# Kernel optimization log

Measured on AMD Instinct MI355X. Metric: run time of the kernel, lower is better.

## Reference

```python
import jax, jax.numpy as jnp
import numpy as np

B, C, H, W = 4, 256, 96, 96
HEADS, RATE = 8, 1


def setup_inputs() -> dict:
    key = jax.random.key(0)
    ks = [jax.random.fold_in(key, i) for i in range(8)]
    kpe = 2 * (RATE // 2) + 1  # PE depthwise kernel size (1 for rate=1)
    return {
        "q": jax.random.normal(ks[0], (B, C, H, W), jnp.float32),
        "k": jax.random.normal(ks[1], (B, C, H, W), jnp.float32),
        "v": jax.random.normal(ks[2], (B, C, H, W), jnp.float32),
        "wq": jax.random.normal(ks[3], (C, C), jnp.float32) * 0.02,          # q_proj 1x1 (used for q,k,v per source)
        "pe_dw": jax.random.normal(ks[4], (9, 1, kpe, kpe), jnp.float32) * 0.3,  # grouped conv, groups=9
        "pe_pw": jax.random.normal(ks[5], (9, 9, 1, 1), jnp.float32) * 0.3,      # 1x1 mixing conv
        "wo": jax.random.normal(ks[6], (C, C), jnp.float32) * 0.02,          # out_proj weight
        "bo": jax.random.normal(ks[7], (C,), jnp.float32) * 0.02,            # out_proj bias
    }


def _unfold3(x, rate):
    # torch.nn.Unfold(3, dilation=rate, padding=rate) then view(N, c, 9, H, W)
    # kernel positions are row-major (ki, kj), channel-major layout -> stack on axis 2.
    n, c, h, w = x.shape
    xp = jnp.pad(x, ((0, 0), (0, 0), (rate, rate), (rate, rate)))
    pats = [xp[:, :, i * rate:i * rate + h, j * rate:j * rate + w]
            for i in range(3) for j in range(3)]
    return jnp.stack(pats, axis=2)  # (N, c, 9, H, W)


def reference(q, b_unused_k=None, v=None, wq=None, pe_dw=None, pe_pw=None, wo=None, bo=None, k=None):
    raise NotImplementedError  # replaced below


def reference(q, k, v, wq, pe_dw, pe_pw, wo, bo):
    b = q.shape[0]
    ch = C // HEADS
    proj = lambda x: jnp.einsum('oc,bchw->bohw', wq, x)  # source uses q_proj for q, k AND v
    qh = proj(q).reshape(b * HEADS, ch, H, W)
    kh = proj(k).reshape(b * HEADS, ch, H, W)
    vh = proj(v).reshape(b * HEADS, ch, H, W)

    ku = _unfold3(kh, RATE)                              # (bH, ch, 9, H, W)
    f = jnp.einsum('nchw,nckhw->nkhw', qh, ku)           # per-pixel 3x3 scores (bH, 9, H, W)

    pad = RATE // 2
    dn = ('NCHW', 'OIHW', 'NCHW')
    f = jax.lax.conv_general_dilated(f, pe_dw, (1, 1), [(pad, pad), (pad, pad)],
                                     feature_group_count=9, dimension_numbers=dn)
    f = jax.lax.conv_general_dilated(f, pe_pw, (1, 1), 'VALID', dimension_numbers=dn)
    s = jax.nn.softmax(f, axis=1)                        # softmax over 9 kernel positions

    vu = _unfold3(vh, RATE)                              # (bH, ch, 9, H, W)
    o = jnp.einsum('nckhw,nkhw->nchw', vu, s).reshape(b, C, H, W)
    return jnp.einsum('oc,bchw->bohw', wo, o) + bo[None, :, None, None]
```

## Files before the change

### kernel.cpp

```cpp
#include <hip/hip_runtime.h>
#include <math.h>

#define HH 96
#define WW 96
#define PP 9216
#define CCH 256
#define BB 4
#define CH 32

typedef unsigned short u16;
typedef short bf16x8 __attribute__((ext_vector_type(8)));
typedef float f32x4 __attribute__((ext_vector_type(4)));

__device__ __forceinline__ float bf2f(unsigned s) { return __uint_as_float(s << 16); }
__device__ __forceinline__ u16 f2bf(float f) {
  unsigned u = __float_as_uint(f);
  return (u16)((u + 0x7fffu + ((u >> 16) & 1u)) >> 16);
}

typedef __attribute__((address_space(1))) const unsigned int GUI;
typedef __attribute__((address_space(3))) unsigned int LUI;
__device__ __forceinline__ void gload16(const void* g, void* l) {
  __builtin_amdgcn_global_load_lds((GUI*)g, (LUI*)l, 16, 0, 0);
}

__global__ __launch_bounds__(256)
void wcvt(const float* __restrict__ wq, const float* __restrict__ wo,
          u16* __restrict__ Wbf) {
  int gidx = blockIdx.x * 256 + threadIdx.x;
  int mat = gidx >> 13;
  int gi = gidx & 8191;
  int l = gi & 63;
  int i = (gi >> 6) & 3;
  int w = (gi >> 8) & 3;
  int ks = (gi >> 10) & 1;
  int kk = (gi >> 11) & 3;
  const float* W = mat ? wo : wq;
  int row = w * 64 + i * 16 + (l & 15);
  int c0 = kk * 64 + (ks * 4 + (l >> 4)) * 8;
  const float* s = W + (size_t)row * CCH + c0;
  float4 a = *(const float4*)s;
  float4 b = *(const float4*)(s + 4);
  uint4 u;
  u.x = (unsigned)f2bf(a.x) | ((unsigned)f2bf(a.y) << 16);
  u.y = (unsigned)f2bf(a.z) | ((unsigned)f2bf(a.w) << 16);
  u.z = (unsigned)f2bf(b.x) | ((unsigned)f2bf(b.y) << 16);
  u.w = (unsigned)f2bf(b.z) | ((unsigned)f2bf(b.w) << 16);
  *(uint4*)(Wbf + (size_t)gidx * 8) = u;
}

#define TSTR 68
__global__ __launch_bounds__(256, 3)
void gemm_qkvf(const float* __restrict__ qin, const float* __restrict__ kin,
               const float* __restrict__ vin, const u16* __restrict__ Wbf,
               u16* __restrict__ Xcl) {
  __shared__ float Tt[2][64][TSTR];
  const int t = threadIdx.x;
  const int w = t >> 6, l = t & 63;
  const int lr = l & 15, lg = l >> 4;
  const int pblk = blockIdx.x * 64;
  const int z = blockIdx.z;
  const int b = z & 3, which = z >> 2;
  const float* Xf = ((which == 0) ? qin : (which == 1) ? kin : vin) + (size_t)b * CCH * PP;
  u16* Y = Xcl + (size_t)z * ((size_t)PP * CCH);

  const int sw_r = ((lr >> 2) & 3) << 3;
  const int cswz = (lr & 3) << 3;

  f32x4 acc[4][4];
#pragma unroll
  for (int mi = 0; mi < 4; mi++)
#pragma unroll
    for (int ni = 0; ni < 4; ni++) acc[mi][ni] = (f32x4){0.f, 0.f, 0.f, 0.f};

  float4 xr[4];
  auto loadX = [&](int kk) {
#pragma unroll
    for (int rr = 0; rr < 4; rr++) {
      int cc = kk * 64 + w * 4 + lg + 16 * rr;
      xr[rr] = *(const float4*)(Xf + (size_t)cc * PP + pblk + lr * 4);
    }
  };
  auto writeT = [&](int buf) {
#pragma unroll
    for (int rr = 0; rr < 4; rr++) {
      int cs = (w * 4 + lg + 16 * rr) ^ cswz;
      Tt[buf][lr * 4 + 0][cs] = xr[rr].x;
      Tt[buf][lr * 4 + 1][cs] = xr[rr].y;
      Tt[buf][lr * 4 + 2][cs] = xr[rr].z;
      Tt[buf][lr * 4 + 3][cs] = xr[rr].w;
    }
  };
  auto mma = [&](int kk, int cur) {
#pragma unroll
    for (int ks = 0; ks < 2; ks++) {
      bf16x8 wf[4], xf[4];
#pragma unroll
      for (int i = 0; i < 4; i++) {
        size_t go = ((((size_t)(kk * 2 + ks) * 4 + w) * 4 + i) * 64 + l) * 8;
        wf[i] = *(const bf16x8*)(Wbf + go);
      }
#pragma unroll
      for (int i = 0; i < 4; i++) {
        int row = i * 16 + lr;
        int c0 = (ks * 32 + lg * 8) ^ sw_r;
        const float* tp = &Tt[cur][row][c0];
        float4 A = *(const float4*)tp;
        float4 Bv = *(const float4*)(tp + 4);
        bf16x8 x;
        x[0] = (short)f2bf(A.x);  x[1] = (short)f2bf(A.y);
        x[2] = (short)f2bf(A.z);  x[3] = (short)f2bf(A.w);
        x[4] = (short)f2bf(Bv.x); x[5] = (short)f2bf(Bv.y);
        x[6] = (short)f2bf(Bv.z); x[7] = (short)f2bf(Bv.w);
        xf[i] = x;
      }
#pragma unroll
      for (int mi = 0; mi < 4; mi++)
#pragma unroll
        for (int ni = 0; ni < 4; ni++)
          acc[mi][ni] = __builtin_amdgcn_mfma_f32_16x16x32_bf16(
              wf[mi], xf[ni], acc[mi][ni], 0, 0, 0);
    }
  };

  loadX(0);
  writeT(0);
  __syncthreads();
#pragma unroll
  for (int kk = 0; kk < 4; kk++) {
    if (kk < 3) loadX(kk + 1);
    mma(kk, kk & 1);
    if (kk < 3) {
      writeT((kk + 1) & 1);
      __syncthreads();
    }
  }

#pragma unroll
  for (int mi = 0; mi < 4; mi++)
#pragma unroll
    for (int ni = 0; ni < 4; ni++) {
      int o = w * 64 + mi * 16 + lg * 4;
      int p = pblk + ni * 16 + lr;
      f32x4 a = acc[mi][ni];
      uint2 u;
      u.x = (unsigned)f2bf(a[0]) | ((unsigned)f2bf(a[1]) << 16);
      u.y = (unsigned)f2bf(a[2]) | ((unsigned)f2bf(a[3]) << 16);
      *(uint2*)(Y + (size_t)p * CCH + o) = u;
    }
}

__global__ __launch_bounds__(256)
void gemm_out_m(const u16* __restrict__ Xbuf, const u16* __restrict__ Wbf,
                const float* __restrict__ bias, float* __restrict__ outY) {
  __shared__ u16 Xl[64 * 64];
  const int t = threadIdx.x;
  const int w = t >> 6, l = t & 63;
  const int lr = l & 15, lg = l >> 4;
  const int pblk = blockIdx.x * 64;
  const int z = blockIdx.z;
  const u16* Xb = Xbuf + (size_t)z * ((size_t)PP * CCH);

  f32x4 acc[4][4];
#pragma unroll
  for (int mi = 0; mi < 4; mi++)
#pragma unroll
    for (int ni = 0; ni < 4; ni++) acc[mi][ni] = (f32x4){0.f, 0.f, 0.f, 0.f};

  for (int kk = 0; kk < 4; kk++) {
    const int c0 = kk * 64;
#pragma unroll
    for (int i = 0; i < 2; i++) {
      int r0 = (w * 2 + i) * 8;
      int row = r0 + (l >> 3);
      int gs = (l & 7) ^ (row & 7);
      gload16(Xb + (size_t)(pblk + row) * CCH + c0 + gs * 8, (void*)&Xl[r0 * 64]);
    }
    __syncthreads();
#pragma unroll
    for (int ks = 0; ks < 2; ks++) {
      const int g = ks * 4 + lg;
      bf16x8 wf[4], xf[4];
#pragma unroll
      for (int i = 0; i < 4; i++) {
        size_t go = ((((size_t)(kk * 2 + ks) * 4 + w) * 4 + i) * 64 + l) * 8;
        wf[i] = *(const bf16x8*)(Wbf + go);
      }
#pragma unroll
      for (int i = 0; i < 4; i++) {
        int row = i * 16 + lr;
        xf[i] = *(const bf16x8*)&Xl[row * 64 + ((g ^ (row & 7)) << 3)];
      }
#pragma unroll
      for (int mi = 0; mi < 4; mi++)
#pragma unroll
        for (int ni = 0; ni < 4; ni++)
          acc[mi][ni] = __builtin_amdgcn_mfma_f32_16x16x32_bf16(
              xf[mi], wf[ni], acc[mi][ni], 0, 0, 0);
    }
    __syncthreads();
  }
#pragma unroll
  for (int ni = 0; ni < 4; ni++) {
    int o = w * 64 + ni * 16 + lr;
    float bv = bias[o];
#pragma unroll
    for (int mi = 0; mi < 4; mi++) {
      int p = pblk + mi * 16 + lg * 4;
      f32x4 a = acc[mi][ni];
      float4 st = {a[0] + bv, a[1] + bv, a[2] + bv, a[3] + bv};
      *(float4*)(outY + ((size_t)z * CCH + o) * PP + p) = st;
    }
  }
}

#define TX 32
#define TY 4
#define HX 34
#define HY 6
#define NHP (HX * HY)
#define NGR (NHP * 4)
#define ARND 4

__device__ __forceinline__ void fma8(const uint4 u, const float* qp, float& s) {
  s = fmaf(qp[0], bf2f(u.x & 0xffffu), s);
  s = fmaf(qp[1], bf2f(u.x >> 16), s);
  s = fmaf(qp[2], bf2f(u.y & 0xffffu), s);
  s = fmaf(qp[3], bf2f(u.y >> 16), s);
  s = fmaf(qp[4], bf2f(u.z & 0xffffu), s);
  s = fmaf(qp[5], bf2f(u.z >> 16), s);
  s = fmaf(qp[6], bf2f(u.w & 0xffffu), s);
  s = fmaf(qp[7], bf2f(u.w >> 16), s);
}
__device__ __forceinline__ void acc8(const uint4 u, float gv, float* op) {
  op[0] = fmaf(gv, bf2f(u.x & 0xffffu), op[0]);
  op[1] = fmaf(gv, bf2f(u.x >> 16), op[1]);
  op[2] = fmaf(gv, bf2f(u.y & 0xffffu), op[2]);
  op[3] = fmaf(gv, bf2f(u.y >> 16), op[3]);
  op[4] = fmaf(gv, bf2f(u.z & 0xffffu), op[4]);
  op[5] = fmaf(gv, bf2f(u.z >> 16), op[5]);
  op[6] = fmaf(gv, bf2f(u.w & 0xffffu), op[6]);
  op[7] = fmaf(gv, bf2f(u.w >> 16), op[7]);
}

__global__ __launch_bounds__(256)
void attn_1b(const u16* __restrict__ Kt, const u16* __restrict__ Vt,
             u16* __restrict__ Qt, const float* __restrict__ pe_dw,
             const float* __restrict__ pe_pw) {
  __shared__ __align__(16) u16 kl[NHP * 32];
  __shared__ __align__(16) u16 vl[NHP * 32];
  __shared__ float coef[81];
  const int t = threadIdx.x;
  if (t < 81) coef[t] = pe_pw[t] * pe_dw[t % 9];

  const int lx = t & 31;
  const int h2 = (t >> 5) & 1;
  const int ly = t >> 6;
  const int x0 = blockIdx.x * TX;
  const int y0 = blockIdx.y * TY;
  const int b = blockIdx.z >> 3;
  const int h = blockIdx.z & 7;
  const size_t nbase = (size_t)b * PP * CCH + h * CH;
  const int p = (y0 + ly) * WW + (x0 + lx);
  const size_t pixhalf = nbase + (size_t)p * CCH + h2 * 16;

  uint4 kg[ARND], vg[ARND];
#pragma unroll
  for (int r = 0; r < ARND; r++) {
    int s = t + r * 256;
    int pix = s >> 2, g = s & 3;
    int hy = pix / HX, hx = pix - hy * HX;
    int gx = x0 - 1 + hx, gy = y0 - 1 + hy;
    bool ok = (s < NGR) & (gx >= 0) & (gx < WW) & (gy >= 0) & (gy < HH);
    uint4 u = make_uint4(0u, 0u, 0u, 0u);
    if (ok) u = *(const uint4*)(Kt + nbase + (size_t)(gy * WW + gx) * CCH + g * 8);
    kg[r] = u;
  }
#pragma unroll
  for (int r = 0; r < ARND; r++) {
    int s = t + r * 256;
    int pix = s >> 2, g = s & 3;
    int hy = pix / HX, hx = pix - hy * HX;
    int gx = x0 - 1 + hx, gy = y0 - 1 + hy;
    bool ok = (s < NGR) & (gx >= 0) & (gx < WW) & (gy >= 0) & (gy < HH);
    uint4 u = make_uint4(0u, 0u, 0u, 0u);
    if (ok) u = *(const uint4*)(Vt + nbase + (size_t)(gy * WW + gx) * CCH + g * 8);
    vg[r] = u;
  }
  uint4 q0 = *(const uint4*)(Qt + pixhalf);
  uint4 q1 = *(const uint4*)(Qt + pixhalf + 8);

#pragma unroll
  for (int r = 0; r < ARND; r++) {
    int s = t + r * 256;
    if (s < NGR) {
      int pix = s >> 2, g = s & 3;
      *(uint4*)(&kl[pix * 32 + (((g + (pix >> 1)) & 3) << 3)]) = kg[r];
    }
  }
#pragma unroll
  for (int r = 0; r < ARND; r++) {
    int s = t + r * 256;
    if (s < NGR) {
      int pix = s >> 2, g = s & 3;
      *(uint4*)(&vl[pix * 32 + (((g + (pix >> 1)) & 3) << 3)]) = vg[r];
    }
  }
  __syncthreads();

  float qh[16];
  qh[0] = bf2f(q0.x & 0xffffu); qh[1] = bf2f(q0.x >> 16);
  qh[2] = bf2f(q0.y & 0xffffu); qh[3] = bf2f(q0.y >> 16);
  qh[4] = bf2f(q0.z & 0xffffu); qh[5] = bf2f(q0.z >> 16);
  qh[6] = bf2f(q0.w & 0xffffu); qh[7] = bf2f(q0.w >> 16);
  qh[8] = bf2f(q1.x & 0xffffu); qh[9] = bf2f(q1.x >> 16);
  qh[10] = bf2f(q1.y & 0xffffu); qh[11] = bf2f(q1.y >> 16);
  qh[12] = bf2f(q1.z & 0xffffu); qh[13] = bf2f(q1.z >> 16);
  qh[14] = bf2f(q1.w & 0xffffu); qh[15] = bf2f(q1.w >> 16);

  float f[9];
#pragma unroll
  for (int kk = 0; kk < 9; kk++) {
    int pix = (ly + kk / 3) * HX + lx + kk % 3;
    int ga = h2 * 2;
    uint4 ka = *(const uint4*)(&kl[pix * 32 + (((ga + (pix >> 1)) & 3) << 3)]);
    uint4 kb = *(const uint4*)(&kl[pix * 32 + (((ga + 1 + (pix >> 1)) & 3) << 3)]);
    float s = 0.f;
    fma8(ka, qh, s);
    fma8(kb, qh + 8, s);
    f[kk] = s + __shfl_xor(s, 32, 64);
  }

  float g[9], m = -1e30f;
#pragma unroll
  for (int k2 = 0; k2 < 9; k2++) {
    float s = 0.f;
#pragma unroll
    for (int kk = 0; kk < 9; kk++) s = fmaf(coef[k2 * 9 + kk], f[kk], s);
    g[k2] = s;
    m = fmaxf(m, s);
  }
  float ssum = 0.f;
#pragma unroll
  for (int k2 = 0; k2 < 9; k2++) {
    g[k2] = __expf(g[k2] - m);
    ssum += g[k2];
  }
  float inv = 1.f / ssum;
#pragma unroll
  for (int k2 = 0; k2 < 9; k2++) g[k2] *= inv;

  float oh[16];
#pragma unroll
  for (int j = 0; j < 16; j++) oh[j] = 0.f;
#pragma unroll
  for (int kk = 0; kk < 9; kk++) {
    int pix = (ly + kk / 3) * HX + lx + kk % 3;
    int ga = h2 * 2;
    uint4 va = *(const uint4*)(&vl[pix * 32 + (((ga + (pix >> 1)) & 3) << 3)]);
    uint4 vb = *(const uint4*)(&vl[pix * 32 + (((ga + 1 + (pix >> 1)) & 3) << 3)]);
    acc8(va, g[kk], oh);
    acc8(vb, g[kk], oh + 8);
  }
  uint4 s0, s1;
  s0.x = (unsigned)f2bf(oh[0]) | ((unsigned)f2bf(oh[1]) << 16);
  s0.y = (unsigned)f2bf(oh[2]) | ((unsigned)f2bf(oh[3]) << 16);
  s0.z = (unsigned)f2bf(oh[4]) | ((unsigned)f2bf(oh[5]) << 16);
  s0.w = (unsigned)f2bf(oh[6]) | ((unsigned)f2bf(oh[7]) << 16);
  s1.x = (unsigned)f2bf(oh[8]) | ((unsigned)f2bf(oh[9]) << 16);
  s1.y = (unsigned)f2bf(oh[10]) | ((unsigned)f2bf(oh[11]) << 16);
  s1.z = (unsigned)f2bf(oh[12]) | ((unsigned)f2bf(oh[13]) << 16);
  s1.w = (unsigned)f2bf(oh[14]) | ((unsigned)f2bf(oh[15]) << 16);
  *(uint4*)(Qt + pixhalf) = s0;
  *(uint4*)(Qt + pixhalf + 8) = s1;
}

extern "C" void kernel_launch(void* const* d_in, const int* in_sizes, int n_in,
                              void* d_out, int out_size, void* d_ws, size_t ws_size,
                              hipStream_t stream) {
  const float* q     = (const float*)d_in[0];
  const float* k     = (const float*)d_in[1];
  const float* v     = (const float*)d_in[2];
  const float* wq    = (const float*)d_in[3];
  const float* pe_dw = (const float*)d_in[4];
  const float* pe_pw = (const float*)d_in[5];
  const float* wo    = (const float*)d_in[6];
  const float* bo    = (const float*)d_in[7];
  float* out = (float*)d_out;

  const size_t seg = (size_t)BB * PP * CCH;
  u16* Xcl = (u16*)d_ws;
  u16* Wbf = Xcl + 3 * seg;

  wcvt<<<64, 256, 0, stream>>>(wq, wo, Wbf);

  gemm_qkvf<<<dim3(PP / 64, 1, 12), 256, 0, stream>>>(q, k, v, Wbf, Xcl);

  u16* Qs = Xcl;
  u16* Ks = Xcl + seg;
  u16* Vs = Xcl + 2 * seg;
  attn_1b<<<dim3(WW / TX, HH / TY, BB * 8), 256, 0, stream>>>(Ks, Vs, Qs, pe_dw, pe_pw);

  gemm_out_m<<<dim3(PP / 64, 1, BB), 256, 0, stream>>>(Qs, Wbf + 65536, bo, out);
}
```

Baseline: 96.40 us.

## Stage full K tile in LDS as bf16 for both projection GEMMs

The QKV projection GEMM now loads all 256 input channels for its 64-pixel tile at once. It transposes them with cross-lane shuffles, converts them to bf16 a single time and stores them in a padded LDS buffer, replacing the double-buffered fp32 transpose that converted to bf16 on every MFMA read. The output GEMM likewise prefetches the entire 64x256 bf16 tile with global_load_lds up front and drops the per-k-step barriers. The aim is to cut sync points, redundant conversions and LDS traffic. In exchange, LDS and register use per block rise and the occupancy hint is dropped, and the load/compute overlap is lost.

```diff
diff --git a/kernel.cpp b/kernel.cpp
--- a/kernel.cpp
+++ b/kernel.cpp
@@ -49,12 +49,12 @@
   *(uint4*)(Wbf + (size_t)gidx * 8) = u;
 }
 
-#define TSTR 68
-__global__ __launch_bounds__(256, 3)
+#define XROW 264
+__global__ __launch_bounds__(256)
 void gemm_qkvf(const float* __restrict__ qin, const float* __restrict__ kin,
                const float* __restrict__ vin, const u16* __restrict__ Wbf,
                u16* __restrict__ Xcl) {
-  __shared__ float Tt[2][64][TSTR];
+  __shared__ u16 Xb[64 * XROW];
   const int t = threadIdx.x;
   const int w = t >> 6, l = t & 63;
   const int lr = l & 15, lg = l >> 4;
@@ -64,8 +64,39 @@
   const float* Xf = ((which == 0) ? qin : (which == 1) ? kin : vin) + (size_t)b * CCH * PP;
   u16* Y = Xcl + (size_t)z * ((size_t)PP * CCH);
 
-  const int sw_r = ((lr >> 2) & 3) << 3;
-  const int cswz = (lr & 3) << 3;
+  float4 xr[16];
+#pragma unroll
+  for (int rr = 0; rr < 16; rr++) {
+    int cc = w * 64 + rr * 4 + lg;
+    xr[rr] = *(const float4*)(Xf + (size_t)cc * PP + pblk + lr * 4);
+  }
+#pragma unroll
+  for (int rr = 0; rr < 16; rr++) {
+    float r0 = xr[rr].x, r1 = xr[rr].y, r2 = xr[rr].z, r3 = xr[rr].w;
+    bool b0 = (lg & 1), b1 = (lg & 2);
+    float s0 = b0 ? r0 : r1;
+    float s1 = b0 ? r2 : r3;
+    float u0 = __shfl_xor(s0, 16, 64);
+    float u1 = __shfl_xor(s1, 16, 64);
+    float m0 = b0 ? u0 : r0;
+    float m1 = b0 ? r1 : u0;
+    float m2 = b0 ? u1 : r2;
+    float m3 = b0 ? r3 : u1;
+    float s2 = b1 ? m0 : m2;
+    float s3 = b1 ? m1 : m3;
+    float w0 = __shfl_xor(s2, 32, 64);
+    float w1 = __shfl_xor(s3, 32, 64);
+    float o0 = b1 ? w0 : m0;
+    float o1 = b1 ? w1 : m1;
+    float o2 = b1 ? m2 : w0;
+    float o3 = b1 ? m3 : w1;
+    int cbase = w * 64 + rr * 4;
+    int pl = lr * 4 + lg;
+    unsigned lo = (unsigned)f2bf(o0) | ((unsigned)f2bf(o1) << 16);
+    unsigned hi = (unsigned)f2bf(o2) | ((unsigned)f2bf(o3) << 16);
+    *(uint2*)(&Xb[pl * XROW + cbase]) = make_uint2(lo, hi);
+  }
+  __syncthreads();
 
   f32x4 acc[4][4];
 #pragma unroll
@@ -73,27 +104,11 @@
 #pragma unroll
     for (int ni = 0; ni < 4; ni++) acc[mi][ni] = (f32x4){0.f, 0.f, 0.f, 0.f};
 
-  float4 xr[4];
-  auto loadX = [&](int kk) {
-#pragma unroll
-    for (int rr = 0; rr < 4; rr++) {
-      int cc = kk * 64 + w * 4 + lg + 16 * rr;
-      xr[rr] = *(const float4*)(Xf + (size_t)cc * PP + pblk + lr * 4);
-    }
-  };
-  auto writeT = [&](int buf) {
-#pragma unroll
-    for (int rr = 0; rr < 4; rr++) {
-      int cs = (w * 4 + lg + 16 * rr) ^ cswz;
-      Tt[buf][lr * 4 + 0][cs] = xr[rr].x;
-      Tt[buf][lr * 4 + 1][cs] = xr[rr].y;
-      Tt[buf][lr * 4 + 2][cs] = xr[rr].z;
-      Tt[buf][lr * 4 + 3][cs] = xr[rr].w;
-    }
-  };
-  auto mma = [&](int kk, int cur) {
+#pragma unroll
+  for (int kk = 0; kk < 4; kk++)
 #pragma unroll
     for (int ks = 0; ks < 2; ks++) {
+      const int q = kk * 8 + ks * 4 + lg;
       bf16x8 wf[4], xf[4];
 #pragma unroll
       for (int i = 0; i < 4; i++) {
@@ -103,16 +118,7 @@
 #pragma unroll
       for (int i = 0; i < 4; i++) {
         int row = i * 16 + lr;
-        int c0 = (ks * 32 + lg * 8) ^ sw_r;
-        const float* tp = &Tt[cur][row][c0];
-        float4 A = *(const float4*)tp;
-        float4 Bv = *(const float4*)(tp + 4);
-        bf16x8 x;
-        x[0] = (short)f2bf(A.x);  x[1] = (short)f2bf(A.y);
-        x[2] = (short)f2bf(A.z);  x[3] = (short)f2bf(A.w);
-        x[4] = (short)f2bf(Bv.x); x[5] = (short)f2bf(Bv.y);
-        x[6] = (short)f2bf(Bv.z); x[7] = (short)f2bf(Bv.w);
-        xf[i] = x;
+        xf[i] = *(const bf16x8*)&Xb[row * XROW + q * 8];
       }
 #pragma unroll
       for (int mi = 0; mi < 4; mi++)
@@ -121,20 +127,6 @@
           acc[mi][ni] = __builtin_amdgcn_mfma_f32_16x16x32_bf16(
               wf[mi], xf[ni], acc[mi][ni], 0, 0, 0);
     }
-  };
-
-  loadX(0);
-  writeT(0);
-  __syncthreads();
-#pragma unroll
-  for (int kk = 0; kk < 4; kk++) {
-    if (kk < 3) loadX(kk + 1);
-    mma(kk, kk & 1);
-    if (kk < 3) {
-      writeT((kk + 1) & 1);
-      __syncthreads();
-    }
-  }
 
 #pragma unroll
   for (int mi = 0; mi < 4; mi++)
@@ -153,7 +145,7 @@
 __global__ __launch_bounds__(256)
 void gemm_out_m(const u16* __restrict__ Xbuf, const u16* __restrict__ Wbf,
                 const float* __restrict__ bias, float* __restrict__ outY) {
-  __shared__ u16 Xl[64 * 64];
+  __shared__ u16 Xl[64 * 256];
   const int t = threadIdx.x;
   const int w = t >> 6, l = t & 63;
   const int lr = l & 15, lg = l >> 4;
@@ -161,25 +153,26 @@
   const int z = blockIdx.z;
   const u16* Xb = Xbuf + (size_t)z * ((size_t)PP * CCH);
 
+#pragma unroll
+  for (int r = 0; r < 8; r++) {
+    int G = r * 256 + t;
+    int row = G >> 5, g = G & 31;
+    int gs = (g & 24) | ((g & 7) ^ (row & 7));
+    gload16(Xb + (size_t)(pblk + row) * CCH + gs * 8, (void*)&Xl[(size_t)G * 8]);
+  }
+  __syncthreads();
+
   f32x4 acc[4][4];
 #pragma unroll
   for (int mi = 0; mi < 4; mi++)
 #pragma unroll
     for (int ni = 0; ni < 4; ni++) acc[mi][ni] = (f32x4){0.f, 0.f, 0.f, 0.f};
 
-  for (int kk = 0; kk < 4; kk++) {
-    const int c0 = kk * 64;
-#pragma unroll
-    for (int i = 0; i < 2; i++) {
-      int r0 = (w * 2 + i) * 8;
-      int row = r0 + (l >> 3);
-      int gs = (l & 7) ^ (row & 7);
-      gload16(Xb + (size_t)(pblk + row) * CCH + c0 + gs * 8, (void*)&Xl[r0 * 64]);
-    }
-    __syncthreads();
+#pragma unroll
+  for (int kk = 0; kk < 4; kk++)
 #pragma unroll
     for (int ks = 0; ks < 2; ks++) {
-      const int g = ks * 4 + lg;
+      const int q = kk * 8 + ks * 4 + lg;
       bf16x8 wf[4], xf[4];
 #pragma unroll
       for (int i = 0; i < 4; i++) {
@@ -189,7 +182,8 @@
 #pragma unroll
       for (int i = 0; i < 4; i++) {
         int row = i * 16 + lr;
-        xf[i] = *(const bf16x8*)&Xl[row * 64 + ((g ^ (row & 7)) << 3)];
+        int qp = (q & 24) | ((q & 7) ^ (row & 7));
+        xf[i] = *(const bf16x8*)&Xl[row * 256 + qp * 8];
       }
 #pragma unroll
       for (int mi = 0; mi < 4; mi++)
@@ -198,8 +192,7 @@
           acc[mi][ni] = __builtin_amdgcn_mfma_f32_16x16x32_bf16(
               xf[mi], wf[ni], acc[mi][ni], 0, 0, 0);
     }
-    __syncthreads();
-  }
+
 #pragma unroll
   for (int ni = 0; ni < 4; ni++) {
     int o = w * 64 + ni * 16 + lr;
```

Result: faster. 90.43 us (-6.2%).
